# Kernel tuning notes

Hardware: AMD Instinct MI355X
Metric: run time of the kernel (lower is better)

## Reference

```python
import jax, jax.numpy as jnp
import numpy as np

FLOAT_EPS = float(np.finfo(np.float32).eps)  # matches torch.finfo(torch.float32).eps


def setup_inputs() -> dict:
    key = jax.random.key(0)
    k0, k1, k2, k3, k4 = jax.random.split(key, 5)
    B, P, I, O, L = 16, 8192, 256, 128, 256  # batch, points, in_shapes, out_shapes, RNN_LATENT_SIZE
    x = jax.random.uniform(k0, (B, P, I), dtype=jnp.float32)
    latent_vector = jax.random.normal(k1, (B, L), dtype=jnp.float32)
    comp1 = 0.1 * jax.random.normal(k2, (L, I, O), dtype=jnp.float32)  # nn.init.normal_(std=0.1)
    comp2 = 0.1 * jax.random.normal(k3, (L, I, O), dtype=jnp.float32)
    temperature = jnp.full((1,), 2.0, dtype=jnp.float32)  # init.constant_(2)
    u = jax.random.uniform(k4, (B, 2, 1, I, O), dtype=jnp.float32)  # gumbel base noise (rand_like)
    return {"x": x, "latent_vector": latent_vector, "comp1": comp1,
            "comp2": comp2, "temperature": temperature, "u": u}


def reference(x, latent_vector, comp1, comp2, temperature, u):
    # mask_l/r: [B, I, O], softmax over the in-shapes axis (dim=-2)
    mask_l = jax.nn.softmax(jnp.einsum('bl,lio->bio', latent_vector, comp1), axis=-2)
    mask_r = jax.nn.softmax(jnp.einsum('bl,lio->bio', latent_vector, comp2), axis=-2)
    mask = jnp.stack([mask_l, mask_r], axis=1)[:, :, None]  # [B, 2, 1, I, O]

    # gumbel-softmax sampling: temperature clamp(eps, 2) then clamp_min(0.001)
    temp = jnp.maximum(jnp.clip(temperature, FLOAT_EPS, 2.0), 0.001)  # shape (1,)
    g = -jnp.log(-jnp.log(jnp.maximum(u, FLOAT_EPS)))
    mask_s = jax.nn.softmax((jnp.log(mask + FLOAT_EPS) + g) / temp, axis=-2)  # [B,2,1,I,O]

    # select: per-head broadcast-multiply-reduce == batched GEMM [B,P,I] x [B,2,I,O]
    sel = jnp.einsum('bpi,bkio->bpko', x, mask_s[:, :, 0])  # [B, P, 2, O]
    a, b = sel[:, :, 0], sel[:, :, 1]

    # arithmetic combine (union, intersection-ish, diffs) + clamp
    out = jnp.concatenate([a + b, a + b - 1.0, a - b, b - a], axis=-1)  # [B, P, 4*O]
    return jnp.clip(out, 0.0, 1.0)
```

## Files before the change

kernel.cpp:

```cpp
#include <hip/hip_runtime.h>
#include <hip/hip_bf16.h>

#define FLOAT_EPS 1.1920928955078125e-07f

typedef float f32x4 __attribute__((ext_vector_type(4)));
typedef short s16x8 __attribute__((ext_vector_type(8)));

#define B_ 16
#define P_ 8192
#define I_ 256
#define O_ 128
#define L_ 256
#define IO_ (I_*O_)

__device__ __forceinline__ float clip01(float v) {
    return fminf(fmaxf(v, 0.0f), 1.0f);
}
__device__ __forceinline__ f32x4 clip01v(f32x4 v) {
    f32x4 r;
    r[0] = clip01(v[0]); r[1] = clip01(v[1]);
    r[2] = clip01(v[2]); r[3] = clip01(v[3]);
    return r;
}

__global__ __launch_bounds__(256) void rl_k1_logits(
        const float* __restrict__ lat,
        const float* __restrict__ c1, const float* __restrict__ c2,
        float* __restrict__ lgP) {
    const int n  = blockIdx.x * 256 + threadIdx.x;
    const int ks = blockIdx.y;
    const int lh = blockIdx.z;
    const float* __restrict__ C  = (ks ? c2 : c1) + (size_t)lh * 128 * IO_;
    const int lbase = lh * 128;

    float acc[16];
#pragma unroll
    for (int b = 0; b < 16; ++b) acc[b] = 0.0f;

#pragma unroll 4
    for (int l = 0; l < 128; ++l) {
        float cv = C[(size_t)l * IO_ + n];
#pragma unroll
        for (int b = 0; b < 16; ++b)
            acc[b] += lat[b * L_ + lbase + l] * cv;
    }
    float* o = lgP + ((size_t)(lh * 32 + ks * 16)) * IO_ + n;
#pragma unroll
    for (int b = 0; b < 16; ++b) o[(size_t)b * IO_] = acc[b];
}

__global__ __launch_bounds__(256) void rl_k2_mask(
        const float* __restrict__ lgP, const float* __restrict__ u,
        const float* __restrict__ temp_p, __hip_bfloat16* __restrict__ MTF) {
    const int oo = threadIdx.x & 15;
    const int g  = threadIdx.x >> 4;
    const int o0 = blockIdx.x * 16;
    const int ks = blockIdx.y;
    const int b  = blockIdx.z;

    __shared__ float slab[I_][16];
    __shared__ float red[16][16];

    const float* __restrict__ z0 = lgP + (size_t)(ks * 16 + b) * IO_ + o0 + oo;
    const float* __restrict__ z1 = z0 + (size_t)32 * IO_;
    const float* __restrict__ up = u + ((size_t)b * 2 + ks) * IO_ + o0 + oo;

    float T = temp_p[0];
    T = fminf(fmaxf(T, FLOAT_EPS), 2.0f);
    T = fmaxf(T, 0.001f);
    const float rT = 1.0f / T;

    const int i0 = g * 16, i1 = i0 + 16;

    for (int i = i0; i < i1; ++i)
        slab[i][oo] = z0[(size_t)i * O_] + z1[(size_t)i * O_];
    __syncthreads();

    float m = -INFINITY;
    for (int i = i0; i < i1; ++i) m = fmaxf(m, slab[i][oo]);
    red[g][oo] = m; __syncthreads();
    m = -INFINITY;
#pragma unroll
    for (int j = 0; j < 16; ++j) m = fmaxf(m, red[j][oo]);
    __syncthreads();

    float S = 0.0f;
    for (int i = i0; i < i1; ++i) S += expf(slab[i][oo] - m);
    red[g][oo] = S; __syncthreads();
    S = 0.0f;
#pragma unroll
    for (int j = 0; j < 16; ++j) S += red[j][oo];
    __syncthreads();
    const float invS = 1.0f / S;

    float m2 = -INFINITY;
    for (int i = i0; i < i1; ++i) {
        float p  = expf(slab[i][oo] - m) * invS;
        float uu = fmaxf(up[(size_t)i * O_], FLOAT_EPS);
        float gg = -logf(-logf(uu));
        float s  = (logf(p + FLOAT_EPS) + gg) * rT;
        slab[i][oo] = s;
        m2 = fmaxf(m2, s);
    }
    red[g][oo] = m2; __syncthreads();
    m2 = -INFINITY;
#pragma unroll
    for (int j = 0; j < 16; ++j) m2 = fmaxf(m2, red[j][oo]);
    __syncthreads();

    float S2 = 0.0f;
    for (int i = i0; i < i1; ++i) S2 += expf(slab[i][oo] - m2);
    red[g][oo] = S2; __syncthreads();
    S2 = 0.0f;
#pragma unroll
    for (int j = 0; j < 16; ++j) S2 += red[j][oo];
    const float invS2 = 1.0f / S2;

    const int n  = ks * 128 + o0 + oo;
    const int f  = n >> 4;
    const int j0 = (f * 8 + (g >> 1)) * 64 + (g & 1) * 32 + oo;
    s16x8* __restrict__ MTFb = (s16x8*)MTF + (size_t)b * 8192;

    union { s16x8 v; __hip_bfloat162 h[4]; } c0, c1;
#pragma unroll
    for (int e = 0; e < 8; e += 2) {
        float v0 = expf(slab[i0 + e][oo]     - m2) * invS2;
        float v1 = expf(slab[i0 + e + 1][oo] - m2) * invS2;
        c0.h[e >> 1] = __float22bfloat162_rn(make_float2(v0, v1));
        float w0 = expf(slab[i0 + 8 + e][oo]     - m2) * invS2;
        float w1 = expf(slab[i0 + 8 + e + 1][oo] - m2) * invS2;
        c1.h[e >> 1] = __float22bfloat162_rn(make_float2(w0, w1));
    }
    MTFb[j0]      = c0.v;
    MTFb[j0 + 16] = c1.v;
}

__global__ __launch_bounds__(512, 2) void rl_k3_gemm(
        const float* __restrict__ X, const __hip_bfloat16* __restrict__ MTF,
        float* __restrict__ OUT) {
    const int tid  = threadIdx.x;
    const int lane = tid & 63, wid = tid >> 6;
    const int b    = blockIdx.y;

    __shared__ s16x8 BF[8192];

    const float* __restrict__ Xb    = X + (size_t)b * P_ * I_;
    const s16x8* __restrict__ MTFb  = (const s16x8*)MTF + (size_t)b * 8192;
    float* __restrict__ Ob          = OUT + (size_t)b * P_ * 512;

    const int l15 = lane & 15, lhi = lane >> 4;
    const int rowbase = blockIdx.x * 512 + wid * 64 + l15;

#pragma unroll
    for (int it = 0; it < 16; ++it) {
        int j = it * 512 + tid;
        BF[j] = MTFb[j];
    }

    float4 raw[16];
    {
        const float* s0 = Xb + (size_t)rowbase * I_ + lhi * 8;
#pragma unroll
        for (int kk = 0; kk < 8; ++kk) {
            raw[2 * kk]     = *(const float4*)(s0 + kk * 32);
            raw[2 * kk + 1] = *(const float4*)(s0 + kk * 32 + 4);
        }
    }
    __syncthreads();

    for (int c = 0; c < 4; ++c) {
        s16x8 af[8];
#pragma unroll
        for (int kk = 0; kk < 8; ++kk) {
            float4 f0 = raw[2 * kk], f1 = raw[2 * kk + 1];
            union { s16x8 v; __hip_bfloat162 h[4]; } cv;
            cv.h[0] = __float22bfloat162_rn(make_float2(f0.x, f0.y));
            cv.h[1] = __float22bfloat162_rn(make_float2(f0.z, f0.w));
            cv.h[2] = __float22bfloat162_rn(make_float2(f1.x, f1.y));
            cv.h[3] = __float22bfloat162_rn(make_float2(f1.z, f1.w));
            af[kk] = cv.v;
        }
        if (c < 3) {
            const float* s1 = Xb + (size_t)(rowbase + (c + 1) * 16) * I_ + lhi * 8;
#pragma unroll
            for (int kk = 0; kk < 8; ++kk) {
                raw[2 * kk]     = *(const float4*)(s1 + kk * 32);
                raw[2 * kk + 1] = *(const float4*)(s1 + kk * 32 + 4);
            }
        }
        __builtin_amdgcn_sched_barrier(0);

        const int prow = blockIdx.x * 512 + wid * 64 + c * 16 + l15;
        float* __restrict__ oprow = Ob + (size_t)prow * 512 + lhi * 4;

#pragma unroll
        for (int fn = 0; fn < 8; ++fn) {
            f32x4 acc_a = (f32x4){0.f, 0.f, 0.f, 0.f};
            f32x4 acc_b = (f32x4){0.f, 0.f, 0.f, 0.f};
            const s16x8* pA = BF + (fn * 8) * 64 + lane;
            const s16x8* pB = BF + ((fn + 8) * 8) * 64 + lane;
#pragma unroll
            for (int kk = 0; kk < 8; ++kk) {
                s16x8 bfa = pA[kk * 64];
                s16x8 bfb = pB[kk * 64];
                acc_a = __builtin_amdgcn_mfma_f32_16x16x32_bf16(bfa, af[kk], acc_a, 0, 0, 0);
                acc_b = __builtin_amdgcn_mfma_f32_16x16x32_bf16(bfb, af[kk], acc_b, 0, 0, 0);
            }
            f32x4 s = acc_a + acc_b;
            float* op = oprow + fn * 16;
            __builtin_nontemporal_store(clip01v(s),             (f32x4*)(op));
            __builtin_nontemporal_store(clip01v(s - 1.0f),      (f32x4*)(op + 128));
            __builtin_nontemporal_store(clip01v(acc_a - acc_b), (f32x4*)(op + 256));
            __builtin_nontemporal_store(clip01v(acc_b - acc_a), (f32x4*)(op + 384));
        }
    }
}

extern "C" void kernel_launch(void* const* d_in, const int* in_sizes, int n_in,
                              void* d_out, int out_size, void* d_ws, size_t ws_size,
                              hipStream_t stream) {
    const float* x    = (const float*)d_in[0];
    const float* lat  = (const float*)d_in[1];
    const float* c1   = (const float*)d_in[2];
    const float* c2   = (const float*)d_in[3];
    const float* temp = (const float*)d_in[4];
    const float* u    = (const float*)d_in[5];
    float* out = (float*)d_out;

    char* ws = (char*)d_ws;
    float*          lgP = (float*)ws;
    __hip_bfloat16* MTF = (__hip_bfloat16*)(ws + (8 << 20));

    rl_k1_logits<<<dim3(128, 2, 2), 256, 0, stream>>>(lat, c1, c2, lgP);
    rl_k2_mask  <<<dim3(8, 2, 16), 256, 0, stream>>>(lgP, u, temp, MTF);
    rl_k3_gemm  <<<dim3(16, 16), 512, 0, stream>>>(x, MTF, out);
}
```

Measured before the change: 138.5 us.

## Drop LDS staging in GEMM, read mask from global, use smaller blocks

The GEMM kernel no longer copies the whole per-batch bf16 mask (128 KB) into shared memory. Each wave now reads mask fragments straight from global memory, relying on L2/L1 caching. Blocks shrink to 256 threads handling 64 rows each (128x16 grid instead of 16x16), which removes the __syncthreads and the X register prefetch pipeline and uses nontemporal loads for X. This gives more blocks and occupancy and drops the LDS fill latency. In exchange, every wave re-reads the mask through the cache hierarchy, and the loop over output columns is no longer unrolled.

```diff
diff --git a/kernel.cpp b/kernel.cpp
--- a/kernel.cpp
+++ b/kernel.cpp
@@ -135,84 +135,54 @@
     MTFb[j0 + 16] = c1.v;
 }
 
-__global__ __launch_bounds__(512, 2) void rl_k3_gemm(
+__global__ __launch_bounds__(256, 4) void rl_k3_gemm(
         const float* __restrict__ X, const __hip_bfloat16* __restrict__ MTF,
         float* __restrict__ OUT) {
     const int tid  = threadIdx.x;
     const int lane = tid & 63, wid = tid >> 6;
     const int b    = blockIdx.y;
-
-    __shared__ s16x8 BF[8192];
-
-    const float* __restrict__ Xb    = X + (size_t)b * P_ * I_;
-    const s16x8* __restrict__ MTFb  = (const s16x8*)MTF + (size_t)b * 8192;
-    float* __restrict__ Ob          = OUT + (size_t)b * P_ * 512;
-
-    const int l15 = lane & 15, lhi = lane >> 4;
-    const int rowbase = blockIdx.x * 512 + wid * 64 + l15;
-
-#pragma unroll
-    for (int it = 0; it < 16; ++it) {
-        int j = it * 512 + tid;
-        BF[j] = MTFb[j];
-    }
-
-    float4 raw[16];
-    {
-        const float* s0 = Xb + (size_t)rowbase * I_ + lhi * 8;
+    const int l15  = lane & 15, lhi = lane >> 4;
+    const int row0 = blockIdx.x * 64 + wid * 16;
+
+    const float* __restrict__ Xb  = X + (size_t)b * P_ * I_;
+    const s16x8* __restrict__ Bb  = (const s16x8*)MTF + (size_t)b * 8192;
+    float* __restrict__ Ob        = OUT + (size_t)b * P_ * 512;
+
+    const float* s0 = Xb + (size_t)(row0 + l15) * I_ + lhi * 8;
+    s16x8 af[8];
+#pragma unroll
+    for (int kk = 0; kk < 8; ++kk) {
+        f32x4 f0 = __builtin_nontemporal_load((const f32x4*)(s0 + kk * 32));
+        f32x4 f1 = __builtin_nontemporal_load((const f32x4*)(s0 + kk * 32 + 4));
+        union { s16x8 v; __hip_bfloat162 h[4]; } cv;
+        cv.h[0] = __float22bfloat162_rn(make_float2(f0[0], f0[1]));
+        cv.h[1] = __float22bfloat162_rn(make_float2(f0[2], f0[3]));
+        cv.h[2] = __float22bfloat162_rn(make_float2(f1[0], f1[1]));
+        cv.h[3] = __float22bfloat162_rn(make_float2(f1[2], f1[3]));
+        af[kk] = cv.v;
+    }
+
+    float* __restrict__ oprow = Ob + (size_t)(row0 + l15) * 512 + lhi * 4;
+
+#pragma unroll 1
+    for (int fn = 0; fn < 8; ++fn) {
+        const s16x8* pA = Bb + fn * 512 + lane;
+        const s16x8* pB = Bb + (fn + 8) * 512 + lane;
+        f32x4 acc_a = (f32x4){0.f, 0.f, 0.f, 0.f};
+        f32x4 acc_b = (f32x4){0.f, 0.f, 0.f, 0.f};
 #pragma unroll
         for (int kk = 0; kk < 8; ++kk) {
-            raw[2 * kk]     = *(const float4*)(s0 + kk * 32);
-            raw[2 * kk + 1] = *(const float4*)(s0 + kk * 32 + 4);
+            s16x8 bfa = pA[kk * 64];
+            s16x8 bfb = pB[kk * 64];
+            acc_a = __builtin_amdgcn_mfma_f32_16x16x32_bf16(bfa, af[kk], acc_a, 0, 0, 0);
+            acc_b = __builtin_amdgcn_mfma_f32_16x16x32_bf16(bfb, af[kk], acc_b, 0, 0, 0);
         }
-    }
-    __syncthreads();
-
-    for (int c = 0; c < 4; ++c) {
-        s16x8 af[8];
-#pragma unroll
-        for (int kk = 0; kk < 8; ++kk) {
-            float4 f0 = raw[2 * kk], f1 = raw[2 * kk + 1];
-            union { s16x8 v; __hip_bfloat162 h[4]; } cv;
-            cv.h[0] = __float22bfloat162_rn(make_float2(f0.x, f0.y));
-            cv.h[1] = __float22bfloat162_rn(make_float2(f0.z, f0.w));
-            cv.h[2] = __float22bfloat162_rn(make_float2(f1.x, f1.y));
-            cv.h[3] = __float22bfloat162_rn(make_float2(f1.z, f1.w));
-            af[kk] = cv.v;
-        }
-        if (c < 3) {
-            const float* s1 = Xb + (size_t)(rowbase + (c + 1) * 16) * I_ + lhi * 8;
-#pragma unroll
-            for (int kk = 0; kk < 8; ++kk) {
-                raw[2 * kk]     = *(const float4*)(s1 + kk * 32);
-                raw[2 * kk + 1] = *(const float4*)(s1 + kk * 32 + 4);
-            }
-        }
-        __builtin_amdgcn_sched_barrier(0);
-
-        const int prow = blockIdx.x * 512 + wid * 64 + c * 16 + l15;
-        float* __restrict__ oprow = Ob + (size_t)prow * 512 + lhi * 4;
-
-#pragma unroll
-        for (int fn = 0; fn < 8; ++fn) {
-            f32x4 acc_a = (f32x4){0.f, 0.f, 0.f, 0.f};
-            f32x4 acc_b = (f32x4){0.f, 0.f, 0.f, 0.f};
-            const s16x8* pA = BF + (fn * 8) * 64 + lane;
-            const s16x8* pB = BF + ((fn + 8) * 8) * 64 + lane;
-#pragma unroll
-            for (int kk = 0; kk < 8; ++kk) {
-                s16x8 bfa = pA[kk * 64];
-                s16x8 bfb = pB[kk * 64];
-                acc_a = __builtin_amdgcn_mfma_f32_16x16x32_bf16(bfa, af[kk], acc_a, 0, 0, 0);
-                acc_b = __builtin_amdgcn_mfma_f32_16x16x32_bf16(bfb, af[kk], acc_b, 0, 0, 0);
-            }
-            f32x4 s = acc_a + acc_b;
-            float* op = oprow + fn * 16;
-            __builtin_nontemporal_store(clip01v(s),             (f32x4*)(op));
-            __builtin_nontemporal_store(clip01v(s - 1.0f),      (f32x4*)(op + 128));
-            __builtin_nontemporal_store(clip01v(acc_a - acc_b), (f32x4*)(op + 256));
-            __builtin_nontemporal_store(clip01v(acc_b - acc_a), (f32x4*)(op + 384));
-        }
+        f32x4 s = acc_a + acc_b;
+        float* op = oprow + fn * 16;
+        __builtin_nontemporal_store(clip01v(s),             (f32x4*)(op));
+        __builtin_nontemporal_store(clip01v(s - 1.0f),      (f32x4*)(op + 128));
+        __builtin_nontemporal_store(clip01v(acc_a - acc_b), (f32x4*)(op + 256));
+        __builtin_nontemporal_store(clip01v(acc_b - acc_a), (f32x4*)(op + 384));
     }
 }
 
@@ -233,5 +203,5 @@
 
     rl_k1_logits<<<dim3(128, 2, 2), 256, 0, stream>>>(lat, c1, c2, lgP);
     rl_k2_mask  <<<dim3(8, 2, 16), 256, 0, stream>>>(lgP, u, temp, MTF);
-    rl_k3_gemm  <<<dim3(16, 16), 512, 0, stream>>>(x, MTF, out);
-}
+    rl_k3_gemm  <<<dim3(128, 16), 256, 0, stream>>>(x, MTF, out);
+}
```

Result: slower. 187.7 us (+35.5%).
